# Optimization experiments

Hardware: AMD Instinct MI355X
Metric: run time of the kernel (lower is better)

Reference implementation:

```python
import jax, jax.numpy as jnp
import numpy as np

C, V, L, P, E, HM, H, M, B, T = 512, 32000, 2, 2, 8, 1024, 8, 256, 2, 1024
TOPK, RATIO = 2, 0.5


def setup_inputs() -> dict:
    key = jax.random.key(0)
    ks = iter(jax.random.split(key, 64))

    def nrm(shape, s=0.02):
        return (jax.random.normal(next(ks), shape) * s).astype(jnp.float32)

    return {
        "ids": jax.random.randint(next(ks), (B, T), 0, V, dtype=jnp.int32),
        "embed_w": nrm((V, C)),
        "mem": nrm((M, C)),
        "mp_w": nrm((2 * C, C)), "mp_b": jnp.zeros((C,), jnp.float32),
        "qkv_w": nrm((L, P, C, 3 * C)), "qkv_b": jnp.zeros((L, P, 3 * C), jnp.float32),
        "aw_w": nrm((L, P, C, H)), "aw_b": jnp.zeros((L, P, H), jnp.float32),
        "dscale": jnp.ones((L, P), jnp.float32),
        "mg_w": nrm((L, P * C, C)), "mg_b": jnp.zeros((L, C), jnp.float32),
        "ln_g": jnp.ones((L, C), jnp.float32), "ln_b": jnp.zeros((L, C), jnp.float32),
        "gw": nrm((L, C, E)), "gb": jnp.zeros((L, E), jnp.float32),
        "ew1": nrm((L, E, C, HM)), "eb1": jnp.zeros((L, E, HM), jnp.float32),
        "ew2": nrm((L, E, HM, C)), "eb2": jnp.zeros((L, E, C), jnp.float32),
        "q1w": nrm((L, C, 4 * C)), "q1b": jnp.zeros((L, 4 * C), jnp.float32),
        "q2w": nrm((L, 4 * C, 1)), "q2b": jnp.zeros((L, 1), jnp.float32),
        "errw": nrm((L, C, C)), "errb": jnp.zeros((L, C), jnp.float32),
        "ag1w": nrm((2 * C, 4 * C)), "ag1b": jnp.zeros((4 * C,), jnp.float32),
        "ag2w": nrm((4 * C, C)), "ag2b": jnp.zeros((C,), jnp.float32),
        "pscale": jnp.ones((C,), jnp.float32),
        "head_w": nrm((C, V)), "head_b": jnp.zeros((V,), jnp.float32),
    }


def _forward(ids, embed_w, mem, mp_w, mp_b, qkv_w, qkv_b, aw_w, aw_b, dscale,
             mg_w, mg_b, ln_g, ln_b, gw, gb, ew1, eb1, ew2, eb2,
             q1w, q1b, q2w, q2b, errw, errb, ag1w, ag1b, ag2w, ag2b,
             pscale, head_w, head_b):
    b, t = ids.shape
    hd = C // H
    x = embed_w[ids]                                        # [B,T,C] embedding gather
    # DynamicMemoryBank: attention over memory slots, concat retrieved
    en = jnp.einsum('btc,mc->btm', x, mem)
    ret = jnp.einsum('btm,mc->btc', jax.nn.softmax(en, -1), mem)
    x = jnp.concatenate([x, ret], -1) @ mp_w + mp_b         # memory_proj
    for l in range(L):
        x_in = x
        # IterativeReasoningBlock: stacked MetaCognitiveAttention phases
        h = x_in
        prior = None
        outs = []
        for p in range(P):
            qkv = (h @ qkv_w[l, p] + qkv_b[l, p]).reshape(b, t, 3, H, hd)
            q, k, v = (jnp.moveaxis(qkv[:, :, i], 1, 2) for i in range(3))  # [B,H,T,hd]
            aware = (h.mean(1) @ aw_w[l, p] + aw_b[l, p])[:, :, None, None]  # [B,H,1,1]
            attn = jax.nn.softmax(
                jnp.einsum('bhtd,bhsd->bhts', q, k) * (dscale[l, p] * aware), -1)
            if prior is not None:
                attn = attn + 0.3 * prior
            prior = jax.lax.stop_gradient(attn)
            o = jnp.einsum('bhts,bhsd->bthd', attn, v).reshape(b, t, C)
            h = jax.nn.silu(o)
            outs.append(h)
        merged = jnp.concatenate(outs, -1) @ mg_w[l] + mg_b[l]
        z = merged + x_in
        mu = z.mean(-1, keepdims=True)
        xn = (z - mu) / jnp.sqrt(z.var(-1, keepdims=True) + 1e-5) * ln_g[l] + ln_b[l]
        # MoE: softmax gate, top-k routing, combine (dense-equivalent math)
        scores = jax.nn.softmax(xn @ gw[l] + gb[l], -1)     # [B,T,E]
        vals, idx = jax.lax.top_k(scores, TOPK)
        w = jnp.sum(jax.nn.one_hot(idx, E, dtype=xn.dtype) * vals[..., None], axis=-2)
        eh = jnp.einsum('btc,ech->bteh', xn, ew1[l]) + eb1[l]
        eh = eh * jax.nn.silu(eh)                           # swiglu act: x*silu(x)
        ey = jnp.einsum('bteh,ehc->btec', eh, ew2[l]) + eb2[l]
        moe_out = jnp.einsum('btec,bte->btc', ey, w)
        reason = xn + moe_out * RATIO
        # IntrospectionLayer (quality estimator sees detached x)
        quality = jax.nn.sigmoid(
            jax.nn.silu(jax.lax.stop_gradient(x_in) @ q1w[l] + q1b[l]) @ q2w[l] + q2b[l])
        intro = x_in + 0.3 * ((x_in * (1.0 - quality)) @ errw[l] + errb[l])
        # AutonomousLearningGate
        gate = jnp.tanh(
            jax.nn.silu(jnp.concatenate([reason, intro], -1) @ ag1w + ag1b) @ ag2w + ag2b)
        x = reason + gate * pscale * intro
    return x @ head_w + head_b                              # [B,T,V]


def reference(ids, embed_w, mem, mp_w, mp_b, qkv_w, qkv_b, aw_w, aw_b, dscale,
              mg_w, mg_b, ln_g, ln_b, gw, gb, ew1, eb1, ew2, eb2,
              q1w, q1b, q2w, q2b, errw, errb, ag1w, ag1b, ag2w, ag2b,
              pscale, head_w, head_b):
    return _forward(ids, embed_w, mem, mp_w, mp_b, qkv_w, qkv_b, aw_w, aw_b, dscale,
                    mg_w, mg_b, ln_g, ln_b, gw, gb, ew1, eb1, ew2, eb2,
                    q1w, q1b, q2w, q2b, errw, errb, ag1w, ag1b, ag2w, ag2b,
                    pscale, head_w, head_b)
```

## Files before the change

### kernel.cpp

```cpp
#include <hip/hip_runtime.h>


#define NTOK 2048
#define CDIM 512
#define TLEN 1024
#define NB 2
#define NH 8
#define VDIM 32000

typedef __attribute__((ext_vector_type(4))) float f32x4;
typedef __attribute__((ext_vector_type(8))) __bf16 bf16x8;

#define AS1 __attribute__((address_space(1)))
#define AS3 __attribute__((address_space(3)))

__device__ __forceinline__ void g2lds16(const void* g, void* l) {
    __builtin_amdgcn_global_load_lds((const AS1 void*)g, (AS3 void*)l, 16, 0, 0);
}

__global__ __launch_bounds__(256) void gemm_bf16(
    const __bf16* __restrict__ A, int lda,
    const __bf16* __restrict__ B,
    float* __restrict__ C_, int ldc,
    __bf16* __restrict__ Cb, int ldcb,
    const float* __restrict__ bias,
    const float* __restrict__ res, int ldres, float alpha,
    int K, int act)
{
    __shared__ __bf16 As[128 * 32];
    __shared__ __bf16 Bs[128 * 32];
    const int tid = threadIdx.x;
    const int w = tid >> 6, lane = tid & 63;
    const int nwg = gridDim.x;
    const int q = nwg >> 3, r = nwg & 7;
    const int xcd = blockIdx.x & 7, ii = blockIdx.x >> 3;
    const int swz = (xcd < r) ? xcd * (q + 1) + ii : r * (q + 1) + (xcd - r) * q + ii;
    const int m0 = (swz & 15) * 128, n0 = (swz >> 4) * 128;
    const int wr = (w >> 1) * 64, wc = (w & 1) * 64;
    f32x4 acc[4][4] = {};
    const int mrow = lane & 15, kq = (lane >> 4) * 8;
    for (int k0 = 0; k0 < K; k0 += 32) {
#pragma unroll
        for (int i = 0; i < 2; ++i) {
            const int boff = w * 2048 + i * 1024 + lane * 16;
            const int row = boff >> 6;
            const int ke = (boff & 63) >> 1;
            g2lds16(A + (long)(m0 + row) * lda + k0 + ke, (char*)As + (boff - lane * 16));
            g2lds16(B + (long)(n0 + row) * K + k0 + ke, (char*)Bs + (boff - lane * 16));
        }
        __syncthreads();
        bf16x8 af[4], bfr[4];
#pragma unroll
        for (int i = 0; i < 4; ++i)
            af[i] = *(const bf16x8*)(As + (wr + i * 16 + mrow) * 32 + kq);
#pragma unroll
        for (int j = 0; j < 4; ++j)
            bfr[j] = *(const bf16x8*)(Bs + (wc + j * 16 + mrow) * 32 + kq);
#pragma unroll
        for (int i = 0; i < 4; ++i)
#pragma unroll
            for (int j = 0; j < 4; ++j)
                acc[i][j] = __builtin_amdgcn_mfma_f32_16x16x32_bf16(af[i], bfr[j], acc[i][j], 0, 0, 0);
        __syncthreads();
    }
    const int col_l = lane & 15, row_l = (lane >> 4) * 4;
#pragma unroll
    for (int i = 0; i < 4; ++i)
#pragma unroll
        for (int j = 0; j < 4; ++j) {
            const int n = n0 + wc + j * 16 + col_l;
            const float bv = bias ? bias[n] : 0.f;
#pragma unroll
            for (int r2 = 0; r2 < 4; ++r2) {
                const int m = m0 + wr + i * 16 + row_l + r2;
                float v = acc[i][j][r2] + bv;
                if (act == 1) v = v / (1.f + __expf(-v));
                else if (act == 2) v = tanhf(v);
                v *= alpha;
                if (res) v += res[(long)m * ldres + n];
                if (C_) C_[(long)m * ldc + n] = v;
                if (Cb) Cb[(long)m * ldcb + n] = (__bf16)v;
            }
        }
}

__global__ __launch_bounds__(256) void route_k(const int* __restrict__ eidx,
                                               int* __restrict__ offi,
                                               int* __restrict__ list,
                                               int* __restrict__ posmap)
{
    __shared__ int cnt[8], fill[8], seg[9];
    const int t = threadIdx.x;
    if (t < 8) cnt[t] = 0;
    __syncthreads();
    for (int i = t; i < NTOK * 2; i += 256) atomicAdd(&cnt[eidx[i]], 1);
    __syncthreads();
    if (t == 0) {
        int run = 0;
        for (int e = 0; e < 8; ++e) {
            seg[e] = run;
            run += (cnt[e] + 127) & ~127;
        }
        seg[8] = run;
    }
    __syncthreads();
    if (t < 8) fill[t] = seg[t];
    if (t < 9) offi[t] = seg[t];
    __syncthreads();
    for (int i = t; i < NTOK * 2; i += 256) {
        const int e = eidx[i];
        const int g = atomicAdd(&fill[e], 1);
        list[g] = i;
        posmap[i] = g;
    }
    __syncthreads();
#pragma unroll
    for (int e = 0; e < 8; ++e)
        for (int g = seg[e] + cnt[e] + t; g < seg[e + 1]; g += 256) list[g] = 0;
}

__global__ __launch_bounds__(256) void moe_g1_k(
    const __bf16* __restrict__ A,
    const __bf16* __restrict__ Bw,
    const float* __restrict__ eb1l,
    const int* __restrict__ offi,
    const int* __restrict__ list,
    __bf16* __restrict__ EHB)
{
    const int m0 = blockIdx.y * 128;
    if (m0 >= offi[8]) return;
    int e = 0;
    while (e < 7 && offi[e + 1] <= m0) ++e;
    const __bf16* B = Bw + (long)e * (1024 * 512);
    const float* bias = eb1l + e * 1024;
    __shared__ __bf16 As[128 * 32];
    __shared__ __bf16 Bs[128 * 32];
    __shared__ int toks[128];
    const int tid = threadIdx.x;
    if (tid < 128) toks[tid] = list[m0 + tid] >> 1;
    __syncthreads();
    const int w = tid >> 6, lane = tid & 63;
    const int n0 = blockIdx.x * 128;
    const int wr = (w >> 1) * 64, wc = (w & 1) * 64;
    f32x4 acc[4][4] = {};
    const int mrow = lane & 15, kq = (lane >> 4) * 8;
    for (int k0 = 0; k0 < 512; k0 += 32) {
#pragma unroll
        for (int i = 0; i < 2; ++i) {
            const int boff = w * 2048 + i * 1024 + lane * 16;
            const int row = boff >> 6;
            const int ke = (boff & 63) >> 1;
            g2lds16(A + (long)toks[row] * 512 + k0 + ke, (char*)As + (boff - lane * 16));
            g2lds16(B + (long)(n0 + row) * 512 + k0 + ke, (char*)Bs + (boff - lane * 16));
        }
        __syncthreads();
        bf16x8 af[4], bfr[4];
#pragma unroll
        for (int i = 0; i < 4; ++i)
            af[i] = *(const bf16x8*)(As + (wr + i * 16 + mrow) * 32 + kq);
#pragma unroll
        for (int j = 0; j < 4; ++j)
            bfr[j] = *(const bf16x8*)(Bs + (wc + j * 16 + mrow) * 32 + kq);
#pragma unroll
        for (int i = 0; i < 4; ++i)
#pragma unroll
            for (int j = 0; j < 4; ++j)
                acc[i][j] = __builtin_amdgcn_mfma_f32_16x16x32_bf16(af[i], bfr[j], acc[i][j], 0, 0, 0);
        __syncthreads();
    }
    const int col_l = lane & 15, row_l = (lane >> 4) * 4;
#pragma unroll
    for (int i = 0; i < 4; ++i)
#pragma unroll
        for (int j = 0; j < 4; ++j) {
            const int n = n0 + wc + j * 16 + col_l;
            const float bv = bias[n];
#pragma unroll
            for (int r = 0; r < 4; ++r) {
                const int g = m0 + wr + i * 16 + row_l + r;
                const float v = acc[i][j][r] + bv;
                EHB[(long)g * 1024 + n] = (__bf16)(v * v / (1.f + __expf(-v)));
            }
        }
}

__global__ __launch_bounds__(256) void moe_g2_k(
    const __bf16* __restrict__ A,
    const __bf16* __restrict__ Bw,
    const float* __restrict__ eb2l,
    const int* __restrict__ offi,
    float* __restrict__ EYS)
{
    const int m0 = blockIdx.y * 128;
    if (m0 >= offi[8]) return;
    int e = 0;
    while (e < 7 && offi[e + 1] <= m0) ++e;
    const __bf16* B = Bw + (long)e * (512 * 1024);
    const float* bias = eb2l + e * 512;
    __shared__ __bf16 As[128 * 32];
    __shared__ __bf16 Bs[128 * 32];
    const int tid = threadIdx.x;
    const int w = tid >> 6, lane = tid & 63;
    const int n0 = blockIdx.x * 128;
    const int wr = (w >> 1) * 64, wc = (w & 1) * 64;
    f32x4 acc[4][4] = {};
    const int mrow = lane & 15, kq = (lane >> 4) * 8;
    for (int k0 = 0; k0 < 1024; k0 += 32) {
#pragma unroll
        for (int i = 0; i < 2; ++i) {
            const int boff = w * 2048 + i * 1024 + lane * 16;
            const int row = boff >> 6;
            const int ke = (boff & 63) >> 1;
            g2lds16(A + (long)(m0 + row) * 1024 + k0 + ke, (char*)As + (boff - lane * 16));
            g2lds16(B + (long)(n0 + row) * 1024 + k0 + ke, (char*)Bs + (boff - lane * 16));
        }
        __syncthreads();
        bf16x8 af[4], bfr[4];
#pragma unroll
        for (int i = 0; i < 4; ++i)
            af[i] = *(const bf16x8*)(As + (wr + i * 16 + mrow) * 32 + kq);
#pragma unroll
        for (int j = 0; j < 4; ++j)
            bfr[j] = *(const bf16x8*)(Bs + (wc + j * 16 + mrow) * 32 + kq);
#pragma unroll
        for (int i = 0; i < 4; ++i)
#pragma unroll
            for (int j = 0; j < 4; ++j)
                acc[i][j] = __builtin_amdgcn_mfma_f32_16x16x32_bf16(af[i], bfr[j], acc[i][j], 0, 0, 0);
        __syncthreads();
    }
    const int col_l = lane & 15, row_l = (lane >> 4) * 4;
#pragma unroll
    for (int i = 0; i < 4; ++i)
#pragma unroll
        for (int j = 0; j < 4; ++j) {
            const int n = n0 + wc + j * 16 + col_l;
            const float bv = bias[n];
#pragma unroll
            for (int r = 0; r < 4; ++r) {
                const int g = m0 + wr + i * 16 + row_l + r;
                EYS[(long)g * 512 + n] = acc[i][j][r] + bv;
            }
        }
}

__global__ __launch_bounds__(256) void reason2_k(const float* __restrict__ xn,
                                                 const float* __restrict__ EYS,
                                                 const float* __restrict__ wv,
                                                 const int* __restrict__ posmap,
                                                 float* __restrict__ reason)
{
    const long i = (long)blockIdx.x * 256 + threadIdx.x;
    const long n = i >> 9;
    const int c = (int)(i & 511);
    const int g0 = posmap[n * 2], g1 = posmap[n * 2 + 1];
    const float v = wv[n * 2] * EYS[(long)g0 * 512 + c] + wv[n * 2 + 1] * EYS[(long)g1 * 512 + c];
    reason[i] = xn[i] + 0.5f * v;
}

__global__ __launch_bounds__(256) void wtrans_k(const float* __restrict__ W0,
                                                __bf16* __restrict__ Wt0, int K, int N,
                                                long sW, long sD)
{
    const float* W = W0 + (long)blockIdx.z * sW;
    __bf16* Wt = Wt0 + (long)blockIdx.z * sD;
    __shared__ float tile[64][65];
    const int k0 = blockIdx.y * 64, n0 = blockIdx.x * 64;
    const int t = threadIdx.x;
#pragma unroll
    for (int i = 0; i < 4; ++i) {
        const int r = (t >> 4) + i * 16;
        const int c = (t & 15) * 4;
        float4 v = *(const float4*)(W + (long)(k0 + r) * N + n0 + c);
        tile[r][c] = v.x; tile[r][c + 1] = v.y; tile[r][c + 2] = v.z; tile[r][c + 3] = v.w;
    }
    __syncthreads();
#pragma unroll
    for (int i = 0; i < 4; ++i) {
        const int rr = (t >> 4) + i * 16;
        const int cc = (t & 15) * 4;
        __bf16* o = Wt + (long)(n0 + rr) * K + k0 + cc;
        o[0] = (__bf16)tile[cc][rr];
        o[1] = (__bf16)tile[cc + 1][rr];
        o[2] = (__bf16)tile[cc + 2][rr];
        o[3] = (__bf16)tile[cc + 3][rr];
    }
}

__global__ __launch_bounds__(256) void cvta_k(const float* __restrict__ src, int lda, int K,
                                              __bf16* __restrict__ dst)
{
    const int row = blockIdx.x, t = threadIdx.x;
    const float* s = src + (long)row * lda;
    __bf16* d = dst + (long)row * K;
    for (int c = t * 4; c < K; c += 1024) {
        float4 v = *(const float4*)(s + c);
        d[c] = (__bf16)v.x; d[c + 1] = (__bf16)v.y; d[c + 2] = (__bf16)v.z; d[c + 3] = (__bf16)v.w;
    }
}

__global__ __launch_bounds__(256) void embed_k(const int* __restrict__ ids,
                                               const float* __restrict__ ew,
                                               float* __restrict__ x,
                                               __bf16* __restrict__ xb)
{
    const int n = blockIdx.x, t = threadIdx.x;
    const long r = (long)ids[n] * CDIM;
    const float v0 = ew[r + t], v1 = ew[r + 256 + t];
    x[(long)n * CDIM + t]       = v0;
    x[(long)n * CDIM + 256 + t] = v1;
    xb[(long)n * CDIM + t]       = (__bf16)v0;
    xb[(long)n * CDIM + 256 + t] = (__bf16)v1;
}

__global__ __launch_bounds__(256) void smrows_k(const float* __restrict__ a,
                                                __bf16* __restrict__ ob)
{
    const int n = blockIdx.x, t = threadIdx.x;
    __shared__ float rs[256];
    float v = a[(long)n * 256 + t];
    rs[t] = v; __syncthreads();
    for (int o = 128; o; o >>= 1) { if (t < o) rs[t] = fmaxf(rs[t], rs[t + o]); __syncthreads(); }
    const float m = rs[0]; __syncthreads();
    const float e = __expf(v - m);
    rs[t] = e; __syncthreads();
    for (int o = 128; o; o >>= 1) { if (t < o) rs[t] += rs[t + o]; __syncthreads(); }
    ob[(long)n * 256 + t] = (__bf16)(e / rs[0]);
}

__global__ __launch_bounds__(256) void concat_bf_k(const float* __restrict__ a,
                                                   const float* __restrict__ b,
                                                   __bf16* __restrict__ o)
{
    const long i = (long)blockIdx.x * 256 + threadIdx.x;
    const long n = i >> 9;
    const int c = (int)(i & 511);
    o[n * 1024 + c]       = (__bf16)a[i];
    o[n * 1024 + 512 + c] = (__bf16)b[i];
}

__global__ __launch_bounds__(64) void meanp_k(const float* __restrict__ A, int lda,
                                              float* __restrict__ part)
{
    const int bid = blockIdx.x;
    const int ts = bid & 15;
    const int cg = (bid >> 4) & 7;
    const int b  = bid >> 7;
    const int c  = cg * 64 + threadIdx.x;
    const float* p = A + ((long)b * TLEN + ts * 64) * lda + c;
    float s = 0.f;
    for (int t = 0; t < 64; ++t) s += p[(long)t * lda];
    part[(long)ts * 1024 + b * 512 + c] = s;
}
__global__ __launch_bounds__(256) void meanr_k(const float* __restrict__ part,
                                               float* __restrict__ hm)
{
    const int i = blockIdx.x * 256 + threadIdx.x;
    float s = 0.f;
    for (int ts = 0; ts < 16; ++ts) s += part[ts * 1024 + i];
    hm[i] = s * (1.f / 1024.f);
}

__global__ __launch_bounds__(64) void aware_k(const float* __restrict__ hm,
                                              const float* __restrict__ aw_w,
                                              const float* __restrict__ aw_b,
                                              int lp, float* __restrict__ out)
{
    const int t = threadIdx.x;
    if (t < NB * NH) {
        const int b = t >> 3, hh = t & 7;
        const float* W = aw_w + (long)lp * CDIM * NH;
        const float* x = hm + b * CDIM;
        float s = aw_b[lp * NH + hh];
        for (int c = 0; c < CDIM; ++c) s += x[c] * W[c * NH + hh];
        out[t] = s;
    }
}

__global__ __launch_bounds__(256) void qkvprep_k(
    const float* __restrict__ qkv,
    const float* __restrict__ dscale, int lp,
    const float* __restrict__ aware,
    __bf16* __restrict__ QKB, __bf16* __restrict__ KB, __bf16* __restrict__ VTB)
{
    const int bh = blockIdx.x >> 4;
    const int tc = blockIdx.x & 15;
    const int b = bh >> 3, h = bh & 7;
    const int tid = threadIdx.x;
    const float sc = dscale[lp] * aware[bh];
    __shared__ float vt[64][68];
    const int row = tid >> 2, c0 = (tid & 3) * 16;
    const long rbase = ((long)(b * 1024 + tc * 64 + row)) * 1536 + h * 64 + c0;
    {
        bf16x8 qo[2], ko[2];
#pragma unroll
        for (int i = 0; i < 2; ++i)
#pragma unroll
            for (int jj = 0; jj < 2; ++jj) {
                const float4 qq = *(const float4*)(qkv + rbase + (i * 2 + jj) * 4);
                const float4 kk = *(const float4*)(qkv + rbase + 512 + (i * 2 + jj) * 4);
                qo[i][jj * 4 + 0] = (__bf16)(qq.x * sc);
                qo[i][jj * 4 + 1] = (__bf16)(qq.y * sc);
                qo[i][jj * 4 + 2] = (__bf16)(qq.z * sc);
                qo[i][jj * 4 + 3] = (__bf16)(qq.w * sc);
                ko[i][jj * 4 + 0] = (__bf16)kk.x;
                ko[i][jj * 4 + 1] = (__bf16)kk.y;
                ko[i][jj * 4 + 2] = (__bf16)kk.z;
                ko[i][jj * 4 + 3] = (__bf16)kk.w;
            }
        const long obase = (long)bh * 65536 + (long)(tc * 64 + row) * 64 + c0;
        *(bf16x8*)(QKB + obase) = qo[0];
        *(bf16x8*)(QKB + obase + 8) = qo[1];
        *(bf16x8*)(KB + obase) = ko[0];
        *(bf16x8*)(KB + obase + 8) = ko[1];
    }
    {
        const long vbase = ((long)(b * 1024 + tc * 64 + row)) * 1536 + 1024 + h * 64 + c0;
#pragma unroll
        for (int i = 0; i < 4; ++i) {
            const float4 v = *(const float4*)(qkv + vbase + i * 4);
            vt[row][c0 + i * 4 + 0] = v.x;
            vt[row][c0 + i * 4 + 1] = v.y;
            vt[row][c0 + i * 4 + 2] = v.z;
            vt[row][c0 + i * 4 + 3] = v.w;
        }
    }
    __syncthreads();
    {
        const int d = row;
        const int s0 = c0;
        bf16x8 o0, o1;
#pragma unroll
        for (int j = 0; j < 8; ++j) o0[j] = (__bf16)vt[s0 + j][d];
#pragma unroll
        for (int j = 0; j < 8; ++j) o1[j] = (__bf16)vt[s0 + 8 + j][d];
        __bf16* dst = VTB + (long)bh * 65536 + (long)d * 1024 + tc * 64 + s0;
        *(bf16x8*)dst = o0;
        *(bf16x8*)(dst + 8) = o1;
    }
}

#define RB 32
__global__ __launch_bounds__(256) void attn2_k(
    const __bf16* __restrict__ QKB,
    const __bf16* __restrict__ KB,
    const __bf16* __restrict__ VTB,
    __bf16* __restrict__ prior,
    int use_prior,
    float* __restrict__ outs, __bf16* __restrict__ outsb, int out_off)
{
    __shared__ __align__(16) __bf16 qs[RB * 64];
    __shared__ __align__(16) __bf16 kv[2][128 * 64];
    __shared__ __align__(16) __bf16 ss[RB * 1024];
    const int tid = threadIdx.x;
    const int w = tid >> 6, lane = tid & 63;
    const int rb = blockIdx.x & 31;
    const int bh = blockIdx.x >> 5;
    const int b = bh >> 3, h = bh & 7;
    const int t0 = rb * RB;
    const long qkbase = (long)bh * 65536;
    const int mrow = lane & 15, kq = (lane >> 4) * 8;

    {
        const int row = tid >> 3, gl = tid & 7;
        const int gs = gl ^ (row & 7);
        g2lds16(QKB + qkbase + (long)(t0 + row) * 64 + gs * 8,
                (char*)qs + tid * 16 - lane * 16);
    }
    {
        for (int it = 0; it < 4; ++it) {
            const int idx = it * 256 + tid;
            const int row = idx >> 3, gl = idx & 7;
            const int gs = gl ^ (row & 7);
            g2lds16(KB + qkbase + (long)row * 64 + gs * 8,
                    (char*)kv[0] + idx * 16 - lane * 16);
        }
        __syncthreads();
        int buf = 0;
        const int ntb = w * 2;
        for (int c = 0; c < 8; ++c) {
            if (c < 7) {
                const int s0n = (c + 1) * 128;
                for (int it = 0; it < 4; ++it) {
                    const int idx = it * 256 + tid;
                    const int row = idx >> 3, gl = idx & 7;
                    const int gs = gl ^ (row & 7);
                    g2lds16(KB + qkbase + (long)(s0n + row) * 64 + gs * 8,
                            (char*)kv[buf ^ 1] + idx * 16 - lane * 16);
                }
            }
            f32x4 accs[2][2] = {};
#pragma unroll
            for (int k0 = 0; k0 < 64; k0 += 32) {
                bf16x8 aq[2], bk[2];
#pragma unroll
                for (int mt = 0; mt < 2; ++mt) {
                    const int r = mt * 16 + mrow;
                    const int col = k0 + kq;
                    aq[mt] = *(const bf16x8*)(qs + r * 64 + (((col >> 3) ^ (r & 7)) << 3));
                }
#pragma unroll
                for (int j = 0; j < 2; ++j) {
                    const int nl = (ntb + j) * 16 + mrow;
                    const int col = k0 + kq;
                    bk[j] = *(const bf16x8*)(kv[buf] + nl * 64 + (((col >> 3) ^ (nl & 7)) << 3));
                }
#pragma unroll
                for (int mt = 0; mt < 2; ++mt)
#pragma unroll
                    for (int j = 0; j < 2; ++j)
                        accs[mt][j] = __builtin_amdgcn_mfma_f32_16x16x32_bf16(aq[mt], bk[j], accs[mt][j], 0, 0, 0);
            }
            const int col_l = lane & 15, row_l = (lane >> 4) * 4;
#pragma unroll
            for (int mt = 0; mt < 2; ++mt)
#pragma unroll
                for (int j = 0; j < 2; ++j) {
                    const int ccol = c * 128 + (ntb + j) * 16 + col_l;
#pragma unroll
                    for (int r = 0; r < 4; ++r) {
                        const int rr = mt * 16 + row_l + r;
                        ss[rr * 1024 + (((ccol >> 3) ^ (rr & 7)) << 3) + (ccol & 7)] = (__bf16)accs[mt][j][r];
                    }
                }
            __syncthreads();
            buf ^= 1;
        }
    }
    for (int it = 0; it < 4; ++it) {
        const int idx = it * 256 + tid;
        const int d = idx >> 4, gl = idx & 15;
        const int gs = gl ^ (d & 7);
        g2lds16(VTB + (long)bh * 65536 + (long)d * 1024 + gs * 8,
                (char*)kv[0] + idx * 16 - lane * 16);
    }
    {
        const int r = tid >> 3;
        const int li = tid & 7;
        const int rsw = r & 7;
        float mx = -1e30f;
        for (int j = 0; j < 16; ++j) {
            const int c = j * 64 + li * 8;
            bf16x8 v = *(const bf16x8*)(ss + r * 1024 + (((c >> 3) ^ rsw) << 3));
#pragma unroll
            for (int q = 0; q < 8; ++q) mx = fmaxf(mx, (float)v[q]);
        }
        mx = fmaxf(mx, __shfl_xor(mx, 1));
        mx = fmaxf(mx, __shfl_xor(mx, 2));
        mx = fmaxf(mx, __shfl_xor(mx, 4));
        float sum = 0.f;
        for (int j = 0; j < 16; ++j) {
            const int c = j * 64 + li * 8;
            __bf16* p = ss + r * 1024 + (((c >> 3) ^ rsw) << 3);
            bf16x8 v = *(const bf16x8*)p;
            bf16x8 e;
#pragma unroll
            for (int q = 0; q < 8; ++q) {
                const float ev = __expf((float)v[q] - mx);
                sum += ev;
                e[q] = (__bf16)ev;
            }
            *(bf16x8*)p = e;
        }
        sum += __shfl_xor(sum, 1);
        sum += __shfl_xor(sum, 2);
        sum += __shfl_xor(sum, 4);
        const float rinv = 1.f / sum;
        const long pbase = ((long)bh * 1024 + t0 + r) * 1024;
        for (int j = 0; j < 16; ++j) {
            const int c = j * 64 + li * 8;
            __bf16* p = ss + r * 1024 + (((c >> 3) ^ rsw) << 3);
            bf16x8 v = *(const bf16x8*)p;
            bf16x8 o;
            if (use_prior) {
                bf16x8 pr = *(const bf16x8*)(prior + pbase + c);
#pragma unroll
                for (int q = 0; q < 8; ++q)
                    o[q] = (__bf16)((float)v[q] * rinv + 0.3f * (float)pr[q]);
            } else {
#pragma unroll
                for (int q = 0; q < 8; ++q)
                    o[q] = (__bf16)((float)v[q] * rinv);
            }
            *(bf16x8*)p = o;
            *(bf16x8*)(prior + pbase + c) = o;
        }
    }
    __syncthreads();
    {
        f32x4 po[2] = {};
        int buf = 0;
        const int mt = w >> 1;
        const int ntb2 = (w & 1) * 2;
        for (int c = 0; c < 8; ++c) {
            if (c < 7) {
                const int s0n = (c + 1) * 128;
                for (int it = 0; it < 4; ++it) {
                    const int idx = it * 256 + tid;
                    const int d = idx >> 4, gl = idx & 15;
                    const int gs = gl ^ (d & 7);
                    g2lds16(VTB + (long)bh * 65536 + (long)d * 1024 + s0n + gs * 8,
                            (char*)kv[buf ^ 1] + idx * 16 - lane * 16);
                }
            }
#pragma unroll
            for (int ks = 0; ks < 4; ++ks) {
                const int r = mt * 16 + mrow;
                const int cola = c * 128 + ks * 32 + kq;
                bf16x8 pa = *(const bf16x8*)(ss + r * 1024 + (((cola >> 3) ^ (r & 7)) << 3));
                bf16x8 vb[2];
#pragma unroll
                for (int j = 0; j < 2; ++j) {
                    const int d = (ntb2 + j) * 16 + mrow;
                    const int colv = ks * 32 + kq;
                    vb[j] = *(const bf16x8*)(kv[buf] + d * 128 + (((colv >> 3) ^ (d & 7)) << 3));
                }
                po[0] = __builtin_amdgcn_mfma_f32_16x16x32_bf16(pa, vb[0], po[0], 0, 0, 0);
                po[1] = __builtin_amdgcn_mfma_f32_16x16x32_bf16(pa, vb[1], po[1], 0, 0, 0);
            }
            __syncthreads();
            buf ^= 1;
        }
        const int col_l = lane & 15, row_l = (lane >> 4) * 4;
#pragma unroll
        for (int j = 0; j < 2; ++j) {
            const int d = out_off + h * 64 + (ntb2 + j) * 16 + col_l;
#pragma unroll
            for (int r = 0; r < 4; ++r) {
                const int trow = t0 + mt * 16 + row_l + r;
                float v = po[j][r];
                v = v / (1.f + __expf(-v));
                const long oi = ((long)(b * 1024 + trow)) * 1024 + d;
                outs[oi] = v;
                outsb[oi] = (__bf16)v;
            }
        }
    }
}

__global__ __launch_bounds__(256) void ln_k(const float* __restrict__ z,
                                            const float* __restrict__ g,
                                            const float* __restrict__ bb,
                                            float* __restrict__ xn,
                                            __bf16* __restrict__ xnb)
{
    const int n = blockIdx.x, t = threadIdx.x;
    __shared__ float rs[256], rq[256];
    const float v0 = z[(long)n * 512 + t];
    const float v1 = z[(long)n * 512 + 256 + t];
    rs[t] = v0 + v1;
    rq[t] = v0 * v0 + v1 * v1;
    __syncthreads();
    for (int o = 128; o; o >>= 1) {
        if (t < o) { rs[t] += rs[t + o]; rq[t] += rq[t + o]; }
        __syncthreads();
    }
    const float mu = rs[0] * (1.f / 512.f);
    const float var = rq[0] * (1.f / 512.f) - mu * mu;
    const float rstd = rsqrtf(var + 1e-5f);
    const float o0 = (v0 - mu) * rstd * g[t] + bb[t];
    const float o1 = (v1 - mu) * rstd * g[t + 256] + bb[t + 256];
    xn[(long)n * 512 + t]       = o0;
    xn[(long)n * 512 + 256 + t] = o1;
    xnb[(long)n * 512 + t]       = (__bf16)o0;
    xnb[(long)n * 512 + 256 + t] = (__bf16)o1;
}

__global__ __launch_bounds__(64) void gate_k(const float* __restrict__ xn,
                                             const float* __restrict__ gw,
                                             const float* __restrict__ gb,
                                             int l, float* __restrict__ wv,
                                             int* __restrict__ eidx)
{
    const int n = blockIdx.x, t = threadIdx.x;
    const int e = t & 7, ch = t >> 3;
    const float* W = gw + (long)l * CDIM * 8;
    float part = 0.f;
    for (int k = ch * 64; k < ch * 64 + 64; ++k) part += xn[(long)n * CDIM + k] * W[k * 8 + e];
    part += __shfl_xor(part, 8, 64);
    part += __shfl_xor(part, 16, 64);
    part += __shfl_xor(part, 32, 64);
    __shared__ float lg[8];
    if (t < 8) lg[t] = part + gb[l * 8 + t];
    __syncthreads();
    if (t == 0) {
        float m = lg[0];
        for (int i = 1; i < 8; ++i) m = fmaxf(m, lg[i]);
        float p[8], s = 0.f;
        for (int i = 0; i < 8; ++i) { p[i] = __expf(lg[i] - m); s += p[i]; }
        const float inv = 1.f / s;
        int i0 = 0;
        for (int i = 1; i < 8; ++i) if (p[i] > p[i0]) i0 = i;
        int i1 = (i0 == 0) ? 1 : 0;
        for (int i = 0; i < 8; ++i) { if (i == i0) continue; if (p[i] > p[i1]) i1 = i; }
        eidx[n * 2] = i0; eidx[n * 2 + 1] = i1;
        wv[n * 2] = p[i0] * inv; wv[n * 2 + 1] = p[i1] * inv;
    }
}

__global__ __launch_bounds__(256) void qual_k(const __bf16* __restrict__ t1,
                                              const float* __restrict__ q2w,
                                              const float* __restrict__ q2b,
                                              int l, float* __restrict__ qual)
{
    const int n = blockIdx.x, t = threadIdx.x;
    const float* W = q2w + (long)l * 2048;
    float s = 0.f;
    for (int k = t; k < 2048; k += 256) s += (float)t1[(long)n * 2048 + k] * W[k];
    __shared__ float rs[256];
    rs[t] = s; __syncthreads();
    for (int o = 128; o; o >>= 1) { if (t < o) rs[t] += rs[t + o]; __syncthreads(); }
    if (t == 0) {
        const float q = rs[0] + q2b[l];
        qual[n] = 1.f / (1.f + __expf(-q));
    }
}

__global__ __launch_bounds__(256) void xq_k(const float* __restrict__ x_in,
                                            const float* __restrict__ qual,
                                            __bf16* __restrict__ xqb)
{
    const long i = (long)blockIdx.x * 256 + threadIdx.x;
    const long n = i >> 9;
    xqb[i] = (__bf16)(x_in[i] * (1.f - qual[n]));
}

__global__ __launch_bounds__(256) void final_k(const float* __restrict__ reason,
                                               const float* __restrict__ gate,
                                               const float* __restrict__ pscale,
                                               const float* __restrict__ intro,
                                               float* __restrict__ xo,
                                               __bf16* __restrict__ xob)
{
    const long i = (long)blockIdx.x * 256 + threadIdx.x;
    const int c = (int)(i & 511);
    const float v = reason[i] + gate[i] * pscale[c] * intro[i];
    xo[i] = v;
    xob[i] = (__bf16)v;
}

extern "C" void kernel_launch(void* const* d_in, const int* in_sizes, int n_in,
                              void* d_out, int out_size, void* d_ws, size_t ws_size,
                              hipStream_t stream)
{
    (void)in_sizes; (void)n_in; (void)out_size; (void)ws_size;
    const int*   ids     = (const int*)  d_in[0];
    const float* embed_w = (const float*)d_in[1];
    const float* mem     = (const float*)d_in[2];
    const float* mp_w    = (const float*)d_in[3];
    const float* mp_b    = (const float*)d_in[4];
    const float* qkv_w   = (const float*)d_in[5];
    const float* qkv_b   = (const float*)d_in[6];
    const float* aw_w    = (const float*)d_in[7];
    const float* aw_b    = (const float*)d_in[8];
    const float* dscale  = (const float*)d_in[9];
    const float* mg_w    = (const float*)d_in[10];
    const float* mg_b    = (const float*)d_in[11];
    const float* ln_g    = (const float*)d_in[12];
    const float* ln_b    = (const float*)d_in[13];
    const float* gw      = (const float*)d_in[14];
    const float* gb      = (const float*)d_in[15];
    const float* ew1     = (const float*)d_in[16];
    const float* eb1     = (const float*)d_in[17];
    const float* ew2     = (const float*)d_in[18];
    const float* eb2     = (const float*)d_in[19];
    const float* q1w     = (const float*)d_in[20];
    const float* q1b     = (const float*)d_in[21];
    const float* q2w     = (const float*)d_in[22];
    const float* q2b     = (const float*)d_in[23];
    const float* errw    = (const float*)d_in[24];
    const float* errb    = (const float*)d_in[25];
    const float* ag1w    = (const float*)d_in[26];
    const float* ag1b    = (const float*)d_in[27];
    const float* ag2w    = (const float*)d_in[28];
    const float* ag2b    = (const float*)d_in[29];
    const float* pscale  = (const float*)d_in[30];
    const float* head_w  = (const float*)d_in[31];
    const float* head_b  = (const float*)d_in[32];
    float* out = (float*)d_out;
    float* ws  = (float*)d_ws;

    const long NC = (long)NTOK * CDIM;
    float* X0   = ws;
    float* X1   = ws + NC;
    float* RET  = ws + 2 * NC;
    float* QKV  = ws + 5 * NC;
    float* OUTS = ws + 8 * NC;
    float* EN   = ws + 10 * NC;
    float* SM   = ws + 10 * NC + NC / 2;
    float* PART = SM;
    float* HMEAN= SM + 16384;
    float* AWARE= SM + 17408;
    float* QUAL = SM + 17472;
    float* WV   = SM + 19520;
    int*   EIDX = (int*)(SM + 23616);
    int*   OFFI = (int*)(SM + 27712);
    int*   LIST = (int*)(SM + 27728);
    int*   POSMAP = (int*)(SM + 32848);
    float* R      = ws + 11 * NC;
    __bf16* PRIORB = (__bf16*)R;
    float* Z      = R;
    float* XN     = R + NC;
    float* REASON = R + 2 * NC;
    float* INTRO  = R + 3 * NC;
    float* GATEB  = R + 5 * NC;
    __bf16* EHB   = (__bf16*)(R + 6 * NC);
    float* EYS    = R + 9 * NC;

    __bf16* bfw = (__bf16*)(ws + 27 * NC);
    __bf16* WB_mp   = bfw;
    __bf16* WB_qkv  = bfw + 524288;
    __bf16* WB_mg   = bfw + 3670016;
    __bf16* WB_q1   = bfw + 4718592;
    __bf16* WB_err  = bfw + 6815744;
    __bf16* WB_ag1  = bfw + 7340032;
    __bf16* WB_ag2  = bfw + 9437184;
    __bf16* WB_memn = bfw + 10485760;
    __bf16* WB_memt = bfw + 10616832;
    __bf16* WB_head = bfw + 10747904;
    __bf16* QKB = bfw + 27131904;
    __bf16* KB  = QKB + 1048576;
    __bf16* VTB = KB + 1048576;
    __bf16* WB_e1   = bfw + 31326208;
    __bf16* WB_e2   = bfw + 39714816;
    __bf16* X0B   = bfw + 48103424;
    __bf16* X1B   = X0B + 1048576;
    __bf16* XCATB = X1B + 1048576;
    __bf16* OUTSB = XCATB + 2097152;
    __bf16* XNB   = OUTSB + 2097152;
    __bf16* XQB   = XNB + 1048576;
    __bf16* Q1BB  = XQB + 1048576;
    __bf16* ENB   = Q1BB + 4194304;

    auto wtransN = [&](const float* W, __bf16* Wt, int K, int N, int cnt, long sW, long sD) {
        wtrans_k<<<dim3(N / 64, K / 64, cnt), 256, 0, stream>>>(W, Wt, K, N, sW, sD);
    };
    auto gemm = [&](const __bf16* A, int lda, const __bf16* Bm, float* C_, int ldc,
                    __bf16* Cb, int ldcb, const float* bias, const float* res, int ldres,
                    float alpha, int Nn, int K, int act) {
        gemm_bf16<<<(Nn / 128) * 16, 256, 0, stream>>>(
            A, lda, Bm, C_, ldc, Cb, ldcb, bias, res, ldres, alpha, K, act);
    };

    wtransN(mp_w, WB_mp, 1024, 512, 1, 0, 0);
    wtransN(qkv_w, WB_qkv, 512, 1536, 4, 512 * 1536, 1536 * 512);
    wtransN(mg_w, WB_mg, 1024, 512, 2, 1024 * 512, 512 * 1024);
    wtransN(q1w, WB_q1, 512, 2048, 2, 512 * 2048, 2048 * 512);
    wtransN(errw, WB_err, 512, 512, 2, 512 * 512, 512 * 512);
    wtransN(ew1, WB_e1, 512, 1024, 16, 524288, 524288);
    wtransN(ew2, WB_e2, 1024, 512, 16, 524288, 524288);
    wtransN(ag1w, WB_ag1, 1024, 2048, 1, 0, 0);
    wtransN(ag2w, WB_ag2, 2048, 512, 1, 0, 0);
    wtransN(head_w, WB_head, 512, VDIM, 1, 0, 0);
    wtransN(mem, WB_memt, 256, 512, 1, 0, 0);
    cvta_k<<<256, 256, 0, stream>>>(mem, 512, 512, WB_memn);

    embed_k<<<NTOK, 256, 0, stream>>>(ids, embed_w, X0, X0B);
    gemm(X0B, 512, WB_memn, EN, 256, nullptr, 0, nullptr, nullptr, 0, 1.f, 256, 512, 0);
    smrows_k<<<NTOK, 256, 0, stream>>>(EN, ENB);
    gemm(ENB, 256, WB_memt, RET, 512, nullptr, 0, nullptr, nullptr, 0, 1.f, 512, 256, 0);
    concat_bf_k<<<4096, 256, 0, stream>>>(X0, RET, XCATB);
    gemm(XCATB, 1024, WB_mp, X0, 512, X0B, 512, mp_b, nullptr, 0, 1.f, 512, 1024, 0);

    float* xcur = X0;
    float* xalt = X1;
    __bf16* xcurB = X0B;
    __bf16* xaltB = X1B;
    for (int l = 0; l < 2; ++l) {
        for (int p = 0; p < 2; ++p) {
            const int lp = l * 2 + p;
            const float* hptr = (p == 0) ? xcur : OUTS;
            const __bf16* hptrB = (p == 0) ? xcurB : OUTSB;
            const int hlda = (p == 0) ? 512 : 1024;
            gemm(hptrB, hlda, WB_qkv + (long)lp * 1536 * 512, QKV, 1536, nullptr, 0,
                 qkv_b + (long)lp * 1536, nullptr, 0, 1.f, 1536, 512, 0);
            meanp_k<<<256, 64, 0, stream>>>(hptr, hlda, PART);
            meanr_k<<<4, 256, 0, stream>>>(PART, HMEAN);
            aware_k<<<1, 64, 0, stream>>>(HMEAN, aw_w, aw_b, lp, AWARE);
            qkvprep_k<<<256, 256, 0, stream>>>(QKV, dscale, lp, AWARE, QKB, KB, VTB);
            attn2_k<<<512, 256, 0, stream>>>(QKB, KB, VTB, PRIORB,
                                             (p == 1) ? 1 : 0, OUTS, OUTSB, p * CDIM);
        }
        gemm(OUTSB, 1024, WB_mg + (long)l * 512 * 1024, Z, 512, nullptr, 0,
             mg_b + (long)l * 512, xcur, 512, 1.f, 512, 1024, 0);
        ln_k<<<NTOK, 256, 0, stream>>>(Z, ln_g + (long)l * 512, ln_b + (long)l * 512, XN, XNB);
        gate_k<<<NTOK, 64, 0, stream>>>(XN, gw, gb, l, WV, EIDX);
        route_k<<<1, 256, 0, stream>>>(EIDX, OFFI, LIST, POSMAP);
        moe_g1_k<<<dim3(8, 40), 256, 0, stream>>>(XNB, WB_e1 + (long)l * 8 * 524288,
                eb1 + (long)l * 8192, OFFI, LIST, EHB);
        moe_g2_k<<<dim3(4, 40), 256, 0, stream>>>(EHB, WB_e2 + (long)l * 8 * 524288,
                eb2 + (long)l * 4096, OFFI, EYS);
        reason2_k<<<4096, 256, 0, stream>>>(XN, EYS, WV, POSMAP, REASON);
        gemm(xcurB, 512, WB_q1 + (long)l * 2048 * 512, nullptr, 0, Q1BB, 2048,
             q1b + (long)l * 2048, nullptr, 0, 1.f, 2048, 512, 1);
        qual_k<<<NTOK, 256, 0, stream>>>(Q1BB, q2w, q2b, l, QUAL);
        xq_k<<<4096, 256, 0, stream>>>(xcur, QUAL, XQB);
        gemm(XQB, 512, WB_err + (long)l * 512 * 512, INTRO, 512, nullptr, 0,
             errb + (long)l * 512, xcur, 512, 0.3f, 512, 512, 0);
        concat_bf_k<<<4096, 256, 0, stream>>>(REASON, INTRO, XCATB);
        gemm(XCATB, 1024, WB_ag1, nullptr, 0, Q1BB, 2048, ag1b, nullptr, 0, 1.f, 2048, 1024, 1);
        gemm(Q1BB, 2048, WB_ag2, GATEB, 512, nullptr, 0, ag2b, nullptr, 0, 1.f, 512, 2048, 2);
        final_k<<<4096, 256, 0, stream>>>(REASON, GATEB, pscale, INTRO, xalt, xaltB);
        float* tmp = xcur; xcur = xalt; xalt = tmp;
        __bf16* tmpb = xcurB; xcurB = xaltB; xaltB = tmpb;
    }
    gemm(xcurB, 512, WB_head, out, VDIM, nullptr, 0, head_b, nullptr, 0, 1.f, VDIM, 512, 0);
}
```

Baseline: 1.679 ms.

## Add 64x64 GEMM tile for narrow outputs and stage epilogue through LDS

Adds a 64x64-tile GEMM kernel used when N<=512, so narrow GEMMs launch four times as many workgroups and fill more of the GPU's compute units. Both GEMM kernels now write the epilogue through a swizzled LDS buffer and emit coalesced float4 and bf16x4 stores, instead of scattered scalar stores straight from MFMA fragments. The cost is extra LDS round trips and barriers in the epilogue, plus lower data reuse per tile in the small kernel.

```diff
diff --git a/kernel.cpp b/kernel.cpp
--- a/kernel.cpp
+++ b/kernel.cpp
@@ -10,6 +10,7 @@
 
 typedef __attribute__((ext_vector_type(4))) float f32x4;
 typedef __attribute__((ext_vector_type(8))) __bf16 bf16x8;
+typedef __attribute__((ext_vector_type(4))) __bf16 bf16x4;
 
 #define AS1 __attribute__((address_space(1)))
 #define AS3 __attribute__((address_space(3)))
@@ -27,8 +28,10 @@
     const float* __restrict__ res, int ldres, float alpha,
     int K, int act)
 {
-    __shared__ __bf16 As[128 * 32];
-    __shared__ __bf16 Bs[128 * 32];
+    __shared__ __align__(16) char smem[16384];
+    __bf16* As = (__bf16*)smem;
+    __bf16* Bs = (__bf16*)(smem + 8192);
+    float* cs = (float*)smem;
     const int tid = threadIdx.x;
     const int w = tid >> 6, lane = tid & 63;
     const int nwg = gridDim.x;
@@ -65,23 +68,136 @@
     }
     const int col_l = lane & 15, row_l = (lane >> 4) * 4;
 #pragma unroll
-    for (int i = 0; i < 4; ++i)
-#pragma unroll
-        for (int j = 0; j < 4; ++j) {
-            const int n = n0 + wc + j * 16 + col_l;
-            const float bv = bias ? bias[n] : 0.f;
-#pragma unroll
-            for (int r2 = 0; r2 < 4; ++r2) {
-                const int m = m0 + wr + i * 16 + row_l + r2;
-                float v = acc[i][j][r2] + bv;
-                if (act == 1) v = v / (1.f + __expf(-v));
-                else if (act == 2) v = tanhf(v);
-                v *= alpha;
-                if (res) v += res[(long)m * ldres + n];
-                if (C_) C_[(long)m * ldc + n] = v;
-                if (Cb) Cb[(long)m * ldcb + n] = (__bf16)v;
-            }
-        }
+    for (int p = 0; p < 4; ++p) {
+        if ((w >> 1) == (p >> 1)) {
+#pragma unroll
+            for (int iq = 0; iq < 2; ++iq) {
+                const int i = (p & 1) * 2 + iq;
+#pragma unroll
+                for (int j = 0; j < 4; ++j) {
+                    const int n_l = wc + j * 16 + col_l;
+                    const float bv = bias ? bias[n0 + n_l] : 0.f;
+#pragma unroll
+                    for (int r2 = 0; r2 < 4; ++r2) {
+                        const int lr = iq * 16 + row_l + r2;
+                        float v = acc[i][j][r2] + bv;
+                        if (act == 1) v = v / (1.f + __expf(-v));
+                        else if (act == 2) v = tanhf(v);
+                        v *= alpha;
+                        cs[lr * 128 + (n_l ^ (((lr >> 2) & 3) << 4))] = v;
+                    }
+                }
+            }
+        }
+        __syncthreads();
+#pragma unroll
+        for (int it = 0; it < 4; ++it) {
+            const int idx = it * 256 + tid;
+            const int row = idx >> 5, c4f = (idx & 31) << 2;
+            const int m = m0 + p * 32 + row;
+            const int n = n0 + c4f;
+            float4 v = *(const float4*)&cs[row * 128 + (c4f ^ (((row >> 2) & 3) << 4))];
+            if (res) {
+                const float4 rv = *(const float4*)(res + (long)m * ldres + n);
+                v.x += rv.x; v.y += rv.y; v.z += rv.z; v.w += rv.w;
+            }
+            if (C_) *(float4*)(C_ + (long)m * ldc + n) = v;
+            if (Cb) {
+                bf16x4 b4;
+                b4[0] = (__bf16)v.x; b4[1] = (__bf16)v.y;
+                b4[2] = (__bf16)v.z; b4[3] = (__bf16)v.w;
+                *(bf16x4*)(Cb + (long)m * ldcb + n) = b4;
+            }
+        }
+        __syncthreads();
+    }
+}
+
+__global__ __launch_bounds__(256) void gemm64_bf16(
+    const __bf16* __restrict__ A, int lda,
+    const __bf16* __restrict__ B,
+    float* __restrict__ C_, int ldc,
+    __bf16* __restrict__ Cb, int ldcb,
+    const float* __restrict__ bias,
+    const float* __restrict__ res, int ldres, float alpha,
+    int K, int act)
+{
+    __shared__ __align__(16) char smem[8192];
+    __bf16* As = (__bf16*)smem;
+    __bf16* Bs = (__bf16*)(smem + 4096);
+    float* cs = (float*)smem;
+    const int tid = threadIdx.x;
+    const int w = tid >> 6, lane = tid & 63;
+    const int nwg = gridDim.x;
+    const int q = nwg >> 3, r = nwg & 7;
+    const int xcd = blockIdx.x & 7, ii = blockIdx.x >> 3;
+    const int swz = (xcd < r) ? xcd * (q + 1) + ii : r * (q + 1) + (xcd - r) * q + ii;
+    const int m0 = (swz & 31) * 64, n0 = (swz >> 5) * 64;
+    const int wr = (w >> 1) * 32, wc = (w & 1) * 32;
+    f32x4 acc[2][2] = {};
+    const int mrow = lane & 15, kq = (lane >> 4) * 8;
+    const int arow = tid >> 2, ke = (tid & 3) * 8;
+    for (int k0 = 0; k0 < K; k0 += 32) {
+        g2lds16(A + (long)(m0 + arow) * lda + k0 + ke, (char*)As + tid * 16 - lane * 16);
+        g2lds16(B + (long)(n0 + arow) * K + k0 + ke, (char*)Bs + tid * 16 - lane * 16);
+        __syncthreads();
+        bf16x8 af[2], bfr[2];
+#pragma unroll
+        for (int i = 0; i < 2; ++i)
+            af[i] = *(const bf16x8*)(As + (wr + i * 16 + mrow) * 32 + kq);
+#pragma unroll
+        for (int j = 0; j < 2; ++j)
+            bfr[j] = *(const bf16x8*)(Bs + (wc + j * 16 + mrow) * 32 + kq);
+#pragma unroll
+        for (int i = 0; i < 2; ++i)
+#pragma unroll
+            for (int j = 0; j < 2; ++j)
+                acc[i][j] = __builtin_amdgcn_mfma_f32_16x16x32_bf16(af[i], bfr[j], acc[i][j], 0, 0, 0);
+        __syncthreads();
+    }
+    const int col_l = lane & 15, row_l = (lane >> 4) * 4;
+#pragma unroll
+    for (int p = 0; p < 2; ++p) {
+        if ((w >> 1) == p) {
+#pragma unroll
+            for (int i = 0; i < 2; ++i)
+#pragma unroll
+                for (int j = 0; j < 2; ++j) {
+                    const int n_l = wc + j * 16 + col_l;
+                    const float bv = bias ? bias[n0 + n_l] : 0.f;
+#pragma unroll
+                    for (int r2 = 0; r2 < 4; ++r2) {
+                        const int lr = i * 16 + row_l + r2;
+                        float v = acc[i][j][r2] + bv;
+                        if (act == 1) v = v / (1.f + __expf(-v));
+                        else if (act == 2) v = tanhf(v);
+                        v *= alpha;
+                        cs[lr * 64 + (n_l ^ (((lr >> 2) & 3) << 4))] = v;
+                    }
+                }
+        }
+        __syncthreads();
+#pragma unroll
+        for (int it = 0; it < 2; ++it) {
+            const int idx = it * 256 + tid;
+            const int row = idx >> 4, c4f = (idx & 15) << 2;
+            const int m = m0 + p * 32 + row;
+            const int n = n0 + c4f;
+            float4 v = *(const float4*)&cs[row * 64 + (c4f ^ (((row >> 2) & 3) << 4))];
+            if (res) {
+                const float4 rv = *(const float4*)(res + (long)m * ldres + n);
+                v.x += rv.x; v.y += rv.y; v.z += rv.z; v.w += rv.w;
+            }
+            if (C_) *(float4*)(C_ + (long)m * ldc + n) = v;
+            if (Cb) {
+                bf16x4 b4;
+                b4[0] = (__bf16)v.x; b4[1] = (__bf16)v.y;
+                b4[2] = (__bf16)v.z; b4[3] = (__bf16)v.w;
+                *(bf16x4*)(Cb + (long)m * ldcb + n) = b4;
+            }
+        }
+        __syncthreads();
+    }
 }
 
 __global__ __launch_bounds__(256) void route_k(const int* __restrict__ eidx,
@@ -838,8 +954,12 @@
     auto gemm = [&](const __bf16* A, int lda, const __bf16* Bm, float* C_, int ldc,
                     __bf16* Cb, int ldcb, const float* bias, const float* res, int ldres,
                     float alpha, int Nn, int K, int act) {
-        gemm_bf16<<<(Nn / 128) * 16, 256, 0, stream>>>(
-            A, lda, Bm, C_, ldc, Cb, ldcb, bias, res, ldres, alpha, K, act);
+        if (Nn <= 512)
+            gemm64_bf16<<<(Nn / 64) * 32, 256, 0, stream>>>(
+                A, lda, Bm, C_, ldc, Cb, ldcb, bias, res, ldres, alpha, K, act);
+        else
+            gemm_bf16<<<(Nn / 128) * 16, 256, 0, stream>>>(
+                A, lda, Bm, C_, ldc, Cb, ldcb, bias, res, ldres, alpha, K, act);
     };
 
     wtransN(mp_w, WB_mp, 1024, 512, 1, 0, 0);
```

Result: faster. 1.597 ms (-4.9%).
